# Performance work log

Hardware: AMD Instinct MI355X
Metric: run time of the kernel (lower is better)

The kernel has to match this reference:

```python
import jax, jax.numpy as jnp
import numpy as np

NUM_CLASSES = 3
STRIDES = (8, 16, 32)


def _decode(out, stride):
    # out: [B, 5+C, H, W] -> [B, H*W, 5+C] decoded to image coords; also return grid [H*W, 2]
    B, C, H, W = out.shape
    yv, xv = jnp.meshgrid(jnp.arange(H), jnp.arange(W), indexing='ij')
    grid = jnp.stack([xv, yv], -1).reshape(H * W, 2).astype(out.dtype)
    o = out.reshape(B, C, H * W).transpose(0, 2, 1)
    xy = (o[..., :2] + grid[None]) * stride
    wh = jnp.exp(o[..., 2:4]) * stride
    return jnp.concatenate([xy, wh, o[..., 4:]], -1), grid


def _pairwise_iou(gt, pr):
    # gt [G,4], pr [A,4], cxcywh -> iou [G,A]
    tl = jnp.maximum(gt[:, None, :2] - gt[:, None, 2:] / 2, pr[None, :, :2] - pr[None, :, 2:] / 2)
    br = jnp.minimum(gt[:, None, :2] + gt[:, None, 2:] / 2, pr[None, :, :2] + pr[None, :, 2:] / 2)
    en = (tl < br).all(-1).astype(gt.dtype)
    area_i = jnp.prod(br - tl, -1) * en
    area_u = jnp.prod(gt[:, None, 2:], -1) + jnp.prod(pr[None, :, 2:], -1) - area_i
    return area_i / (area_u + 1e-16)


def _iou_loss(pred, target):
    # elementwise IOUloss (loss_type='iou'): 1 - iou^2, shapes [..., 4]
    tl = jnp.maximum(pred[..., :2] - pred[..., 2:] / 2, target[..., :2] - target[..., 2:] / 2)
    br = jnp.minimum(pred[..., :2] + pred[..., 2:] / 2, target[..., :2] + target[..., 2:] / 2)
    en = (tl < br).all(-1).astype(pred.dtype)
    area_i = jnp.prod(br - tl, -1) * en
    area_u = jnp.prod(pred[..., 2:], -1) + jnp.prod(target[..., 2:], -1) - area_i
    iou = area_i / (area_u + 1e-16)
    return 1.0 - iou ** 2


def _bce_logits(x, y):
    # stable BCEWithLogits, reduction='none'
    return jnp.maximum(x, 0) - x * y + jnp.log1p(jnp.exp(-jnp.abs(x)))


def _assign(gt_boxes, gt_cls, box_p, cls_p, obj_p, xs, ys, strides):
    # SimOTA for one image. gt_boxes [G,4], gt_cls [G], box_p [A,4], cls_p [A,C], obj_p [A,1]
    G = gt_boxes.shape[0]
    C = cls_p.shape[-1]
    xc = (xs + 0.5) * strides  # [A] anchor centers in image coords
    yc = (ys + 0.5) * strides
    # anchors inside gt boxes
    gl = gt_boxes[:, 0:1] - gt_boxes[:, 2:3] / 2
    gr = gt_boxes[:, 0:1] + gt_boxes[:, 2:3] / 2
    gt_ = gt_boxes[:, 1:2] - gt_boxes[:, 3:4] / 2
    gb = gt_boxes[:, 1:2] + gt_boxes[:, 3:4] / 2
    in_box = (xc[None] > gl) & (xc[None] < gr) & (yc[None] > gt_) & (yc[None] < gb)  # [G,A]
    # anchors inside center radius 2.5 * stride
    r = 2.5
    in_ctr = ((xc[None] > gt_boxes[:, 0:1] - r * strides[None]) &
              (xc[None] < gt_boxes[:, 0:1] + r * strides[None]) &
              (yc[None] > gt_boxes[:, 1:2] - r * strides[None]) &
              (yc[None] < gt_boxes[:, 1:2] + r * strides[None]))
    cand = in_box.any(0) | in_ctr.any(0)  # [A] candidate anchors (fg_mask)
    in_both = in_box & in_ctr  # [G,A]
    ious = jnp.where(cand[None], _pairwise_iou(gt_boxes, box_p), 0.0)
    iou_cost = -jnp.log(ious + 1e-8)
    p = jnp.sqrt(jax.nn.sigmoid(cls_p) * jax.nn.sigmoid(obj_p))  # [A,C]
    y = jax.nn.one_hot(gt_cls, C, dtype=p.dtype)  # [G,C]
    cls_cost = -(jnp.einsum('gc,ac->ga', y, jnp.log(p + 1e-8)) +
                 jnp.einsum('gc,ac->ga', 1 - y, jnp.log(1 - p + 1e-8)))
    cost = cls_cost + 3.0 * iou_cost + 1e5 * (~in_both).astype(p.dtype)
    cost = jnp.where(cand[None], cost, 1e9)
    # dynamic-k: k_g = clamp(int(sum of top-10 ious), 1)
    topk_ious, _ = jax.lax.top_k(ious, 10)
    dyn_k = jnp.clip(topk_ious.sum(-1).astype(jnp.int32), 1, None)  # [G]
    ranks = jnp.argsort(jnp.argsort(cost, axis=1), axis=1)
    matching = (ranks < dyn_k[:, None]) & cand[None]  # [G,A]
    # resolve anchors matched to multiple gts by min cost
    multi = matching.sum(0) > 1  # [A]
    best = jnp.arange(G)[:, None] == jnp.argmin(cost, axis=0)[None]  # [G,A]
    matching = jnp.where(multi[None], best, matching)
    fg = matching.any(0)  # [A]
    matched_gt = jnp.argmax(matching, axis=0)  # [A]
    pred_iou = (matching.astype(p.dtype) * ious).sum(0)  # [A]
    cls_t = jax.nn.one_hot(gt_cls[matched_gt], C, dtype=p.dtype) * pred_iou[:, None]  # [A,C]
    reg_t = gt_boxes[matched_gt]  # [A,4]
    return fg, cls_t, reg_t


def _forward(p3, p4, p5, mask_inputs, labels, input_images, mask_labels, now_epoch):
    outs, grids, str_list = [], [], []
    for o, s in zip((p3, p4, p5), STRIDES):
        dec, g = _decode(o, float(s))
        outs.append(dec)
        grids.append(g)
        str_list.append(jnp.full((g.shape[0],), float(s), dtype=dec.dtype))
    outputs = jnp.concatenate(outs, 1)  # [B, A, 5+C]
    xs = jnp.concatenate([g[:, 0] for g in grids], 0)  # [A]
    ys = jnp.concatenate([g[:, 1] for g in grids], 0)
    strides = jnp.concatenate(str_list, 0)
    box_p = outputs[..., :4]
    obj_p = outputs[..., 4:5]
    cls_p = outputs[..., 5:]
    gt_boxes = labels[..., :4]
    gt_cls = labels[..., 4].astype(jnp.int32)
    fg, cls_t, reg_t = jax.vmap(_assign, in_axes=(0, 0, 0, 0, 0, None, None, None))(
        gt_boxes, gt_cls, box_p, cls_p, obj_p, xs, ys, strides)
    # assignment is @torch.no_grad() in the original
    fg, cls_t, reg_t = jax.lax.stop_gradient((fg, cls_t, reg_t))
    fgf = fg.astype(outputs.dtype)  # [B,A]
    num_fg = jnp.maximum(fgf.sum(), 1.0)
    loss_iou = (_iou_loss(box_p, reg_t) * fgf).sum()
    loss_obj = _bce_logits(obj_p[..., 0], fgf).sum()
    loss_cls = (_bce_logits(cls_p, cls_t) * fgf[..., None]).sum()
    # segmentation losses: CE (mean NLL over pixels) + Dice
    logp = jax.nn.log_softmax(mask_inputs, axis=1)  # [B,C,H,W]
    ce = -jnp.take_along_axis(logp, mask_labels[:, None].astype(jnp.int32), axis=1).mean()
    sm = jax.nn.softmax(mask_inputs, axis=1).transpose(0, 2, 3, 1)  # [B,H,W,C]
    oh = jax.nn.one_hot(mask_labels, NUM_CLASSES + 1, dtype=sm.dtype)[..., :NUM_CLASSES]
    tp = (oh * sm).sum((0, 1, 2))
    fp = sm.sum((0, 1, 2)) - tp
    fn = oh.sum((0, 1, 2)) - tp
    smooth = 1e-5
    dice = 1.0 - jnp.mean((2 * tp + smooth) / (2 * tp + fn + fp + smooth))  # beta=1
    loss_mask = ce + dice
    loss_sc = jnp.zeros((), outputs.dtype)  # is_sc=False
    reg_w = 5.0
    total = (reg_w * loss_iou + loss_obj + loss_cls + loss_sc) / num_fg + loss_mask
    return jnp.stack([total, reg_w * loss_iou / num_fg, loss_obj / num_fg,
                      loss_cls / num_fg, loss_mask, loss_sc / num_fg])


def setup_inputs() -> dict:
    key = jax.random.key(0)
    ks = jax.random.split(key, 8)
    B, IMG, G = 8, 1024, 20
    C5 = NUM_CLASSES + 5
    p3 = jax.random.normal(ks[0], (B, C5, 128, 128), jnp.float32)
    p4 = jax.random.normal(ks[1], (B, C5, 64, 64), jnp.float32)
    p5 = jax.random.normal(ks[2], (B, C5, 32, 32), jnp.float32)
    mask_inputs = jax.random.normal(ks[3], (B, NUM_CLASSES, IMG, IMG), jnp.float32)
    cxy = jax.random.uniform(ks[4], (B, G, 2), jnp.float32, 64.0, float(IMG - 64))
    wh = jax.random.uniform(ks[5], (B, G, 2), jnp.float32, 16.0, 256.0)
    cls = jax.random.randint(ks[6], (B, G, 1), 0, NUM_CLASSES).astype(jnp.float32)
    labels = jnp.concatenate([cxy, wh, cls], -1)  # [B,G,5] (cx,cy,w,h,class)
    input_images = jax.random.uniform(ks[7], (B, 1, IMG, IMG), jnp.float32)
    mask_labels = jax.random.randint(jax.random.fold_in(key, 9), (B, IMG, IMG), 0, NUM_CLASSES)
    return {"p3": p3, "p4": p4, "p5": p5, "mask_inputs": mask_inputs,
            "labels": labels, "input_images": input_images,
            "mask_labels": mask_labels, "now_epoch": 0}


def reference(p3, p4, p5, mask_inputs, labels, input_images, mask_labels, now_epoch):
    return _forward(p3, p4, p5, mask_inputs, labels, input_images, mask_labels, now_epoch)
```

## Files before the change

kernel.cpp:

```cpp
#include <hip/hip_runtime.h>
#include <cfloat>

constexpr int A_TOT = 21504;
constexpr int NB    = 8;
constexpr int NG    = 20;
constexpr int HW_M  = 1 << 20;
constexpr int SPLIT = 16;
constexpr int CHUNK = A_TOT / SPLIT;
constexpr int MBLK  = 2048;

constexpr float L2E = 1.44269504088896340736f;
constexpr float LN2 = 0.69314718055994530942f;

constexpr size_t OFF_DEC  = 0;
constexpr size_t SZ_DEC   = (size_t)NB * A_TOT * 8;
constexpr size_t OFF_IOUS = OFF_DEC + SZ_DEC;
constexpr size_t SZ_GA    = (size_t)NB * NG * A_TOT;
constexpr size_t OFF_COST = OFF_IOUS + SZ_GA;
constexpr size_t OFF_THRC = OFF_COST + SZ_GA;
constexpr size_t OFF_THRI = OFF_THRC + NB * NG;
constexpr size_t OFF_CAND = OFF_THRI + NB * NG;
constexpr size_t OFF_PM   = OFF_CAND + (NB * A_TOT) / 4;
constexpr size_t OFF_PK   = OFF_PM + 672 * 4;
constexpr size_t OFF_PV   = OFF_PK + (size_t)MBLK * 10;
constexpr size_t SZ_PART  = (size_t)NB * NG * SPLIT * 10;
constexpr size_t OFF_PC   = OFF_PV + SZ_PART;
constexpr size_t OFF_PI   = OFF_PC + SZ_PART;

__device__ __forceinline__ float hw_exp2(float x) { return __builtin_amdgcn_exp2f(x); }
__device__ __forceinline__ float hw_log2(float x) { return __builtin_amdgcn_logf(x); }
__device__ __forceinline__ float fexp(float x) { return hw_exp2(x * L2E); }
__device__ __forceinline__ float flog(float x) { return hw_log2(x) * LN2; }
__device__ __forceinline__ float frcp(float x) { return __builtin_amdgcn_rcpf(x); }
__device__ __forceinline__ float fsig(float x) { return frcp(1.f + fexp(-x)); }
__device__ __forceinline__ float fbce(float x, float y) {
  float t = hw_exp2(-fabsf(x) * L2E);
  return fmaxf(x, 0.f) - x * y + LN2 * hw_log2(1.f + t);
}
__device__ __forceinline__ void anchor_geom(int a, int& hw, int& lw, float& st) {
  if (a < 16384)      { hw = a;         lw = 7; st = 8.f;  }
  else if (a < 20480) { hw = a - 16384; lw = 6; st = 16.f; }
  else                { hw = a - 20480; lw = 5; st = 32.f; }
}

__device__ __forceinline__ void merge_desc(float* a, const float* b) {
  float m[16];
  m[0] = a[0]; m[1] = a[1]; m[2] = a[2]; m[3] = a[3]; m[4] = a[4]; m[5] = a[5];
  m[6] = fmaxf(a[6], b[9]); m[7] = fmaxf(a[7], b[8]);
  m[8] = fmaxf(a[8], b[7]); m[9] = fmaxf(a[9], b[6]);
  m[10] = b[5]; m[11] = b[4]; m[12] = b[3]; m[13] = b[2]; m[14] = b[1]; m[15] = b[0];
#pragma unroll
  for (int s = 8; s >= 1; s >>= 1) {
#pragma unroll
    for (int i = 0; i < 16; ++i) {
      if (!(i & s)) {
        float hi = fmaxf(m[i], m[i + s]);
        float lo = fminf(m[i], m[i + s]);
        m[i] = hi; m[i + s] = lo;
      }
    }
  }
#pragma unroll
  for (int j = 0; j < 10; ++j) a[j] = m[j];
}

__device__ __forceinline__ void merge_asc(float* ac, int* ai,
                                          const float* bc, const int* bi) {
  float mc[16]; int mi[16];
#pragma unroll
  for (int i = 0; i < 6; ++i) { mc[i] = ac[i]; mi[i] = ai[i]; }
#pragma unroll
  for (int i = 6; i < 10; ++i) {
    float c2 = bc[15 - i]; int i2 = bi[15 - i];
    bool ta = (ac[i] < c2) || (ac[i] == c2 && ai[i] < i2);
    mc[i] = ta ? ac[i] : c2; mi[i] = ta ? ai[i] : i2;
  }
  mc[10] = bc[5]; mi[10] = bi[5]; mc[11] = bc[4]; mi[11] = bi[4];
  mc[12] = bc[3]; mi[12] = bi[3]; mc[13] = bc[2]; mi[13] = bi[2];
  mc[14] = bc[1]; mi[14] = bi[1]; mc[15] = bc[0]; mi[15] = bi[0];
#pragma unroll
  for (int s = 8; s >= 1; s >>= 1) {
#pragma unroll
    for (int i = 0; i < 16; ++i) {
      if (!(i & s)) {
        float cA = mc[i], cB = mc[i + s];
        int   iA = mi[i], iB = mi[i + s];
        bool ta = (cB < cA) || (cB == cA && iB < iA);
        mc[i]     = ta ? cB : cA; mi[i]     = ta ? iB : iA;
        mc[i + s] = ta ? cA : cB; mi[i + s] = ta ? iA : iB;
      }
    }
  }
#pragma unroll
  for (int j = 0; j < 10; ++j) { ac[j] = mc[j]; ai[j] = mi[j]; }
}

__global__ __launch_bounds__(256) void k_cost(
    const float* __restrict__ p3, const float* __restrict__ p4,
    const float* __restrict__ p5, const float* __restrict__ labels,
    float* __restrict__ dec, float* __restrict__ ious,
    float* __restrict__ cost, unsigned char* __restrict__ cand) {
  __shared__ float gt[NG][5];
  int tid = threadIdx.x, b = blockIdx.y;
  if (tid < NG * 5) ((float*)gt)[tid] = labels[b * NG * 5 + tid];
  __syncthreads();
  int a = blockIdx.x * 256 + tid;

  int hw, lw; float st;
  anchor_geom(a, hw, lw, st);
  const float* src; int HW;
  if (a < 16384)      { src = p3; HW = 16384; }
  else if (a < 20480) { src = p4; HW = 4096;  }
  else                { src = p5; HW = 1024;  }
  int x = hw & ((1 << lw) - 1), y = hw >> lw;
  const float* c0 = src + (size_t)b * 8 * HW + hw;
  float o0 = c0[0];
  float o1 = c0[(size_t)HW];
  float o2 = c0[(size_t)2 * HW];
  float o3 = c0[(size_t)3 * HW];
  float o4 = c0[(size_t)4 * HW];
  float o5 = c0[(size_t)5 * HW];
  float o6 = c0[(size_t)6 * HW];
  float o7 = c0[(size_t)7 * HW];
  float px = (o0 + (float)x) * st, py = (o1 + (float)y) * st;
  float pw = fexp(o2) * st,        ph = fexp(o3) * st;
  {
    float4* dst = (float4*)(dec + ((size_t)b * A_TOT + a) * 8);
    dst[0] = make_float4(px, py, pw, ph);
    dst[1] = make_float4(o4, o5, o6, o7);
  }

  float xc = ((float)x + 0.5f) * st, yc = ((float)y + 0.5f) * st;

  float so = fsig(o4);
  float cc0, cc1, cc2, S;
  {
    float q0 = sqrtf(fsig(o5) * so);
    float q1 = sqrtf(fsig(o6) * so);
    float q2 = sqrtf(fsig(o7) * so);
    float lg0 = flog(q0 + 1e-8f), lg1 = flog(q1 + 1e-8f), lg2 = flog(q2 + 1e-8f);
    float m0 = flog(1.f - q0 + 1e-8f), m1 = flog(1.f - q1 + 1e-8f), m2 = flog(1.f - q2 + 1e-8f);
    S = m0 + m1 + m2;
    cc0 = lg0 - m0; cc1 = lg1 - m1; cc2 = lg2 - m2;
  }

  float iouv[NG];
  unsigned bothMask = 0;
  bool anyBox = false, anyCtr = false;
  float hpw = pw * 0.5f, hph = ph * 0.5f;
  float plx = px - hpw, prx = px + hpw, pty = py - hph, pby = py + hph;
  float parea = pw * ph;
  float r = 2.5f * st;

#pragma unroll
  for (int g = 0; g < NG; ++g) {
    float gx = gt[g][0], gy = gt[g][1], gw = gt[g][2], gh = gt[g][3];
    float hgw = gw * 0.5f, hgh = gh * 0.5f;
    float glx = gx - hgw, grx = gx + hgw, gty = gy - hgh, gby = gy + hgh;
    bool ib = (xc > glx) && (xc < grx) && (yc > gty) && (yc < gby);
    bool ic = (xc > gx - r) && (xc < gx + r) && (yc > gy - r) && (yc < gy + r);
    anyBox |= ib; anyCtr |= ic;
    if (ib && ic) bothMask |= (1u << g);
    float tlx = fmaxf(glx, plx), brx = fminf(grx, prx);
    float tly = fmaxf(gty, pty), bry = fminf(gby, pby);
    float en = ((tlx < brx) && (tly < bry)) ? 1.f : 0.f;
    float ai = (brx - tlx) * (bry - tly) * en;
    float au = gw * gh + parea - ai;
    iouv[g] = ai / (au + 1e-16f);
  }
  bool cd = anyBox || anyCtr;
  cand[(size_t)b * A_TOT + a] = cd ? 1 : 0;

#pragma unroll
  for (int g = 0; g < NG; ++g) {
    float iv = cd ? iouv[g] : 0.f;
    int cg = (int)gt[g][4];
    float ccg = (cg == 0) ? cc0 : ((cg == 1) ? cc1 : cc2);
    float c = -(ccg + S) - 3.f * flog(iv + 1e-8f) +
              (((bothMask >> g) & 1u) ? 0.f : 100000.f);
    size_t idx = ((size_t)(b * NG + g)) * A_TOT + a;
    ious[idx] = iv;
    cost[idx] = cd ? c : 1e9f;
  }
}

__global__ __launch_bounds__(64) void k_topk_part(
    const float* __restrict__ ious, const float* __restrict__ cost,
    float* __restrict__ pV, float* __restrict__ pC, int* __restrict__ pI) {
  int s = blockIdx.x, g = blockIdx.y, b = blockIdx.z;
  int lane = threadIdx.x;
  int row = b * NG + g;
  int lo = s * CHUNK;
  const float4* iou4 = (const float4*)(ious + (size_t)row * A_TOT + lo);
  const float4* cst4 = (const float4*)(cost + (size_t)row * A_TOT + lo);
  constexpr int NG4 = CHUNK / 4;

  float tv[10];
  float tc[10]; int ti[10];
#pragma unroll
  for (int j = 0; j < 10; ++j) { tv[j] = -1e30f; tc[j] = FLT_MAX; ti[j] = 0x7fffffff; }

  auto insV = [&](float v) {
    if (v > tv[9]) {
#pragma unroll
      for (int j = 0; j < 10; ++j)
        if (v > tv[j]) { float t = tv[j]; tv[j] = v; v = t; }
    }
  };
  auto insC = [&](float c, int ii) {
    if ((c < tc[9]) || (c == tc[9] && ii < ti[9])) {
#pragma unroll
      for (int j = 0; j < 10; ++j) {
        bool lt = (c < tc[j]) || (c == tc[j] && ii < ti[j]);
        if (lt) {
          float t = tc[j]; tc[j] = c; c = t;
          int t2 = ti[j]; ti[j] = ii; ii = t2;
        }
      }
    }
  };

#pragma unroll 1
  for (int grp = lane; grp < NG4; grp += 64) {
    float4 v4 = iou4[grp];
    float4 c4 = cst4[grp];
    int base = lo + grp * 4;
    insV(v4.x); insV(v4.y); insV(v4.z); insV(v4.w);
    insC(c4.x, base); insC(c4.y, base + 1); insC(c4.z, base + 2); insC(c4.w, base + 3);
  }

#pragma unroll 1
  for (int d = 1; d < 64; d <<= 1) {
    float bv[10];
#pragma unroll
    for (int j = 0; j < 10; ++j) bv[j] = __shfl_xor(tv[j], d, 64);
    merge_desc(tv, bv);
  }
#pragma unroll 1
  for (int d = 1; d < 64; d <<= 1) {
    float bc[10]; int bi[10];
#pragma unroll
    for (int j = 0; j < 10; ++j) {
      bc[j] = __shfl_xor(tc[j], d, 64);
      bi[j] = __shfl_xor(ti[j], d, 64);
    }
    merge_asc(tc, ti, bc, bi);
  }

  if (lane == 0) {
    size_t base = ((size_t)row * SPLIT + s) * 10;
#pragma unroll
    for (int j = 0; j < 10; ++j) {
      pV[base + j] = tv[j];
      pC[base + j] = tc[j];
      pI[base + j] = ti[j];
    }
  }
}

__global__ __launch_bounds__(192) void k_topk_merge(
    const float* __restrict__ pV, const float* __restrict__ pC,
    const int* __restrict__ pI, float* __restrict__ thrC, int* __restrict__ thrI) {
  int g = blockIdx.x, b = blockIdx.y, tid = threadIdx.x;
  int row = b * NG + g;
  constexpr int NC = SPLIT * 10;
  __shared__ float sV[NC], sC[NC];
  __shared__ int   sI[NC];
  __shared__ float slot[10];
  __shared__ int kS;

  if (tid < NC) {
    size_t base = (size_t)row * NC + tid;
    sV[tid] = pV[base];
    sC[tid] = pC[base];
    sI[tid] = pI[base];
  }
  __syncthreads();

  float myV = 0.f, myC = 0.f; int myI = 0, rankV = 0;
  if (tid < NC) {
    myV = sV[tid]; myC = sC[tid]; myI = sI[tid];
    for (int j = 0; j < NC; ++j) {
      float v = sV[j];
      rankV += ((v > myV) || (v == myV && j < tid)) ? 1 : 0;
    }
  }
  if (tid < NC && rankV < 10) slot[rankV] = myV;
  __syncthreads();
  if (tid == 0) {
    float sum = 0.f;
#pragma unroll
    for (int j = 0; j < 10; ++j) sum += slot[j];
    int k = (int)sum; if (k < 1) k = 1;
    kS = k;
  }
  __syncthreads();
  if (tid < NC) {
    int rankC = 0;
    for (int j = 0; j < NC; ++j) {
      float c = sC[j];
      rankC += ((c < myC) || (c == myC && sI[j] < myI)) ? 1 : 0;
    }
    if (rankC == kS - 1) { thrC[row] = myC; thrI[row] = myI; }
  }
}

__global__ __launch_bounds__(256) void k_match(
    const float* __restrict__ dec, const float* __restrict__ labels,
    const float* __restrict__ ious, const float* __restrict__ cost,
    const unsigned char* __restrict__ cand,
    const float* __restrict__ thrC, const int* __restrict__ thrI,
    float* __restrict__ pm) {
  __shared__ float gt[NG][5];
  __shared__ float tC[NG];
  __shared__ int   tI[NG];
  int tid = threadIdx.x, b = blockIdx.y;
  if (tid < NG * 5) ((float*)gt)[tid] = labels[b * NG * 5 + tid];
  if (tid >= 128 && tid < 128 + NG) tC[tid - 128] = thrC[b * NG + tid - 128];
  if (tid >= 160 && tid < 160 + NG) tI[tid - 160] = thrI[b * NG + tid - 160];
  __syncthreads();
  int a = blockIdx.x * 256 + tid;

  bool cd = cand[(size_t)b * A_TOT + a] != 0;
  int cnt = 0, firstg = -1, gmin = 0;
  float minc = FLT_MAX, pisum = 0.f, iou_gmin = 0.f;
#pragma unroll
  for (int g = 0; g < NG; ++g) {
    size_t idx = ((size_t)(b * NG + g)) * A_TOT + a;
    float c = cost[idx];
    float iv = ious[idx];
    if (c < minc) { minc = c; gmin = g; iou_gmin = iv; }
    bool m = cd && ((c < tC[g]) || (c == tC[g] && a <= tI[g]));
    if (m) { cnt++; if (firstg < 0) firstg = g; pisum += iv; }
  }
  if (cnt > 1) { firstg = gmin; pisum = iou_gmin; }
  bool fg = cnt > 0;

  const float4* dp = (const float4*)(dec + ((size_t)b * A_TOT + a) * 8);
  float4 d0 = dp[0], d1 = dp[1];
  float l_obj = fbce(d1.x, fg ? 1.f : 0.f);
  float l_iou = 0.f, l_cls = 0.f, nfg = fg ? 1.f : 0.f;
  if (fg) {
    float gx = gt[firstg][0], gy = gt[firstg][1];
    float gw = gt[firstg][2], gh = gt[firstg][3];
    int cg = (int)gt[firstg][4];
    float px = d0.x, py = d0.y, pw = d0.z, ph = d0.w;
    float tlx = fmaxf(px - pw * 0.5f, gx - gw * 0.5f);
    float brx = fminf(px + pw * 0.5f, gx + gw * 0.5f);
    float tly = fmaxf(py - ph * 0.5f, gy - gh * 0.5f);
    float bry = fminf(py + ph * 0.5f, gy + gh * 0.5f);
    float en = ((tlx < brx) && (tly < bry)) ? 1.f : 0.f;
    float ai = (brx - tlx) * (bry - tly) * en;
    float au = pw * ph + gw * gh - ai;
    float iou = ai / (au + 1e-16f);
    l_iou = 1.f - iou * iou;
    l_cls  = fbce(d1.y, (cg == 0) ? pisum : 0.f);
    l_cls += fbce(d1.z, (cg == 1) ? pisum : 0.f);
    l_cls += fbce(d1.w, (cg == 2) ? pisum : 0.f);
  }

  __shared__ float scr[4][4];
  float vals[4] = { nfg, l_iou, l_obj, l_cls };
#pragma unroll
  for (int k = 0; k < 4; ++k) {
    float v = vals[k];
#pragma unroll
    for (int off = 32; off > 0; off >>= 1) v += __shfl_down(v, off, 64);
    if ((tid & 63) == 0) scr[tid >> 6][k] = v;
  }
  __syncthreads();
  if (tid == 0) {
    int bf = blockIdx.y * gridDim.x + blockIdx.x;
#pragma unroll
    for (int k = 0; k < 4; ++k)
      pm[(size_t)bf * 4 + k] = scr[0][k] + scr[1][k] + scr[2][k] + scr[3][k];
  }
}

__global__ __launch_bounds__(256) void k_mask(
    const float* __restrict__ mi, const int* __restrict__ ml,
    float* __restrict__ pk) {
  int tid = threadIdx.x;
  int blk = blockIdx.x;
  int b  = blk >> 8;
  int g0 = (blk & 255) << 10;
  const float* base0 = mi + (size_t)b * 3 * HW_M + (size_t)g0 * 4;
  const int*   lbase = ml + ((size_t)b << 20) + (size_t)g0 * 4;

  float4 x0[4], x1[4], x2[4]; int4 lb[4];
#pragma unroll
  for (int u = 0; u < 4; ++u) {
    size_t off = (size_t)(tid + u * 256) * 4;
    x0[u] = *(const float4*)(base0 + off);
    x1[u] = *(const float4*)(base0 + HW_M + off);
    x2[u] = *(const float4*)(base0 + 2 * HW_M + off);
    lb[u] = *(const int4*)(lbase + off);
  }

  float ce = 0.f, tp0 = 0, tp1 = 0, tp2 = 0;
  float ss0 = 0, ss1 = 0;
  float c0 = 0, c1 = 0;

  auto proc = [&](float v0, float v1, float v2, int l) {
    float e0 = hw_exp2(v0 * L2E);
    float e1 = hw_exp2(v1 * L2E);
    float e2 = hw_exp2(v2 * L2E);
    float sum = e0 + e1 + e2;
    float inv = __builtin_amdgcn_rcpf(sum);
    float lse = hw_log2(sum) * LN2;
    float s0 = e0 * inv, s1 = e1 * inv;
    ss0 += s0; ss1 += s1;
    bool l0 = (l == 0), l1 = (l == 1);
    float vl = l0 ? v0 : (l1 ? v1 : v2);
    float el = l0 ? e0 : (l1 ? e1 : e2);
    float sl = el * inv;
    ce += vl - lse;
    tp0 += l0 ? sl : 0.f;
    tp1 += l1 ? sl : 0.f;
    tp2 += (!l0 && !l1) ? sl : 0.f;
    c0 += l0 ? 1.f : 0.f;
    c1 += l1 ? 1.f : 0.f;
  };

#pragma unroll
  for (int u = 0; u < 4; ++u) {
    proc(x0[u].x, x1[u].x, x2[u].x, lb[u].x);
    proc(x0[u].y, x1[u].y, x2[u].y, lb[u].y);
    proc(x0[u].z, x1[u].z, x2[u].z, lb[u].z);
    proc(x0[u].w, x1[u].w, x2[u].w, lb[u].w);
  }
  float ss2 = 16.f - ss0 - ss1;
  float c2 = 16.f - c0 - c1;

  __shared__ float scr[4][10];
  float vals[10] = { ce, tp0, tp1, tp2, ss0, ss1, ss2, c0, c1, c2 };
#pragma unroll
  for (int k = 0; k < 10; ++k) {
    float v = vals[k];
#pragma unroll
    for (int off = 32; off > 0; off >>= 1) v += __shfl_down(v, off, 64);
    if ((tid & 63) == 0) scr[tid >> 6][k] = v;
  }
  __syncthreads();
  if (tid == 0) {
#pragma unroll
    for (int k = 0; k < 10; ++k)
      pk[(size_t)blk * 10 + k] = scr[0][k] + scr[1][k] + scr[2][k] + scr[3][k];
  }
}

__device__ __forceinline__ float bsum256(float v, float* scr) {
#pragma unroll
  for (int off = 32; off > 0; off >>= 1) v += __shfl_down(v, off, 64);
  __syncthreads();
  if ((threadIdx.x & 63) == 0) scr[threadIdx.x >> 6] = v;
  __syncthreads();
  return scr[0] + scr[1] + scr[2] + scr[3];
}

__global__ __launch_bounds__(256) void k_final(
    const float* __restrict__ pm, const float* __restrict__ pk,
    float* __restrict__ out) {
  __shared__ float scr[4];
  int tid = threadIdx.x;
  float t0 = 0, t1 = 0, t2 = 0, t3 = 0;
  for (int r = tid; r < 672; r += 256) {
    t0 += pm[(size_t)r * 4 + 0];
    t1 += pm[(size_t)r * 4 + 1];
    t2 += pm[(size_t)r * 4 + 2];
    t3 += pm[(size_t)r * 4 + 3];
  }
  float u[10] = {0,0,0,0,0,0,0,0,0,0};
  for (int r = tid; r < MBLK; r += 256) {
#pragma unroll
    for (int k = 0; k < 10; ++k) u[k] += pk[(size_t)r * 10 + k];
  }
  float S_nfg = bsum256(t0, scr);
  float S_iou = bsum256(t1, scr);
  float S_obj = bsum256(t2, scr);
  float S_cls = bsum256(t3, scr);
  float S_ce  = bsum256(u[0], scr);
  float S_tp0 = bsum256(u[1], scr);
  float S_tp1 = bsum256(u[2], scr);
  float S_tp2 = bsum256(u[3], scr);
  float S_ss0 = bsum256(u[4], scr);
  float S_ss1 = bsum256(u[5], scr);
  float S_ss2 = bsum256(u[6], scr);
  float S_c0  = bsum256(u[7], scr);
  float S_c1  = bsum256(u[8], scr);
  float S_c2  = bsum256(u[9], scr);

  if (tid == 0) {
    float nfg = fmaxf(S_nfg, 1.f);
    float o1 = 5.f * S_iou / nfg;
    float o2 = S_obj / nfg;
    float o3 = S_cls / nfg;
    float ce = -S_ce / (float)((long long)NB << 20);
    float tps[3] = { S_tp0, S_tp1, S_tp2 };
    float sss[3] = { S_ss0, S_ss1, S_ss2 };
    float cns[3] = { S_c0, S_c1, S_c2 };
    float ds = 0.f;
#pragma unroll
    for (int c = 0; c < 3; ++c) {
      float tp = tps[c];
      float fp = sss[c] - tp;
      float fn = cns[c] - tp;
      ds += (2.f * tp + 1e-5f) / (2.f * tp + fn + fp + 1e-5f);
    }
    float dice = 1.f - ds / 3.f;
    float o4 = ce + dice;
    out[0] = o1 + o2 + o3 + o4;
    out[1] = o1;
    out[2] = o2;
    out[3] = o3;
    out[4] = o4;
    out[5] = 0.f;
  }
}

extern "C" void kernel_launch(void* const* d_in, const int* in_sizes, int n_in,
                              void* d_out, int out_size, void* d_ws, size_t ws_size,
                              hipStream_t stream) {
  const float* p3     = (const float*)d_in[0];
  const float* p4     = (const float*)d_in[1];
  const float* p5     = (const float*)d_in[2];
  const float* mi     = (const float*)d_in[3];
  const float* labels = (const float*)d_in[4];
  const int*   ml     = (const int*)d_in[6];

  float* ws   = (float*)d_ws;
  float* dec  = ws + OFF_DEC;
  float* ious = ws + OFF_IOUS;
  float* cost = ws + OFF_COST;
  float* thrC = ws + OFF_THRC;
  int*   thrI = (int*)(ws + OFF_THRI);
  unsigned char* cand = (unsigned char*)(ws + OFF_CAND);
  float* pm   = ws + OFF_PM;
  float* pk   = ws + OFF_PK;
  float* pV   = ws + OFF_PV;
  float* pC   = ws + OFF_PC;
  int*   pI   = (int*)(ws + OFF_PI);
  float* out  = (float*)d_out;

  dim3 gA(A_TOT / 256, NB);
  k_cost<<<gA, 256, 0, stream>>>(p3, p4, p5, labels, dec, ious, cost, cand);
  k_topk_part<<<dim3(SPLIT, NG, NB), 64, 0, stream>>>(ious, cost, pV, pC, pI);
  k_topk_merge<<<dim3(NG, NB), 192, 0, stream>>>(pV, pC, pI, thrC, thrI);
  k_match<<<gA, 256, 0, stream>>>(dec, labels, ious, cost, cand, thrC, thrI, pm);
  k_mask<<<MBLK, 256, 0, stream>>>(mi, ml, pk);
  k_final<<<1, 256, 0, stream>>>(pm, pk, out);
}
```

Before: 104.5 us.

## Split independent mask-loss work across the four detection kernels to fill idle CUs

Removes the standalone mask kernel and splits its 2048 blocks into four slices. Each slice rides as extra blocks on one of the detection-loss kernels (cost, top-k partial, top-k merge, match), so the small, latency-bound detection stages share the GPU with bandwidth-heavy mask work instead of leaving CUs idle. The top-k partial kernel also packs four 64-thread wavefronts per 256-thread block. This removes one launch but adds branch divergence between block roles and may raise register or LDS pressure for the fused kernels.

```diff
diff --git a/kernel.cpp b/kernel.cpp
--- a/kernel.cpp
+++ b/kernel.cpp
@@ -8,6 +8,7 @@
 constexpr int SPLIT = 16;
 constexpr int CHUNK = A_TOT / SPLIT;
 constexpr int MBLK  = 2048;
+constexpr int MSLC  = MBLK / 4;
 
 constexpr float L2E = 1.44269504088896340736f;
 constexpr float LN2 = 0.69314718055994530942f;
@@ -95,16 +96,90 @@
   for (int j = 0; j < 10; ++j) { ac[j] = mc[j]; ai[j] = mi[j]; }
 }
 
-__global__ __launch_bounds__(256) void k_cost(
+__device__ __forceinline__ void mask_block(int vblk,
+    const float* __restrict__ mi, const int* __restrict__ ml,
+    float* __restrict__ pk, int tid) {
+  int b  = vblk >> 8;
+  int g0 = (vblk & 255) << 10;
+  const float* base0 = mi + (size_t)b * 3 * HW_M + (size_t)g0 * 4;
+  const int*   lbase = ml + ((size_t)b << 20) + (size_t)g0 * 4;
+
+  float4 x0[4], x1[4], x2[4]; int4 lb[4];
+#pragma unroll
+  for (int u = 0; u < 4; ++u) {
+    size_t off = (size_t)(tid + u * 256) * 4;
+    x0[u] = *(const float4*)(base0 + off);
+    x1[u] = *(const float4*)(base0 + HW_M + off);
+    x2[u] = *(const float4*)(base0 + 2 * HW_M + off);
+    lb[u] = *(const int4*)(lbase + off);
+  }
+
+  float ce = 0.f, tp0 = 0, tp1 = 0, tp2 = 0;
+  float ss0 = 0, ss1 = 0, c0 = 0, c1 = 0;
+
+  auto proc = [&](float v0, float v1, float v2, int l) {
+    float e0 = hw_exp2(v0 * L2E);
+    float e1 = hw_exp2(v1 * L2E);
+    float e2 = hw_exp2(v2 * L2E);
+    float sum = e0 + e1 + e2;
+    float inv = __builtin_amdgcn_rcpf(sum);
+    float lse = hw_log2(sum) * LN2;
+    float s0 = e0 * inv, s1 = e1 * inv;
+    ss0 += s0; ss1 += s1;
+    bool l0 = (l == 0), l1 = (l == 1);
+    float vl = l0 ? v0 : (l1 ? v1 : v2);
+    float el = l0 ? e0 : (l1 ? e1 : e2);
+    float sl = el * inv;
+    ce += vl - lse;
+    tp0 += l0 ? sl : 0.f;
+    tp1 += l1 ? sl : 0.f;
+    tp2 += (!l0 && !l1) ? sl : 0.f;
+    c0 += l0 ? 1.f : 0.f;
+    c1 += l1 ? 1.f : 0.f;
+  };
+
+#pragma unroll
+  for (int u = 0; u < 4; ++u) {
+    proc(x0[u].x, x1[u].x, x2[u].x, lb[u].x);
+    proc(x0[u].y, x1[u].y, x2[u].y, lb[u].y);
+    proc(x0[u].z, x1[u].z, x2[u].z, lb[u].z);
+    proc(x0[u].w, x1[u].w, x2[u].w, lb[u].w);
+  }
+  float ss2 = 16.f - ss0 - ss1;
+  float c2 = 16.f - c0 - c1;
+
+  __shared__ float scr[4][10];
+  float vals[10] = { ce, tp0, tp1, tp2, ss0, ss1, ss2, c0, c1, c2 };
+#pragma unroll
+  for (int k = 0; k < 10; ++k) {
+    float v = vals[k];
+#pragma unroll
+    for (int off = 32; off > 0; off >>= 1) v += __shfl_down(v, off, 64);
+    if ((tid & 63) == 0) scr[tid >> 6][k] = v;
+  }
+  __syncthreads();
+  if (tid == 0) {
+#pragma unroll
+    for (int k = 0; k < 10; ++k)
+      pk[(size_t)vblk * 10 + k] = scr[0][k] + scr[1][k] + scr[2][k] + scr[3][k];
+  }
+}
+
+__global__ __launch_bounds__(256) void k_cost_mask(
     const float* __restrict__ p3, const float* __restrict__ p4,
     const float* __restrict__ p5, const float* __restrict__ labels,
     float* __restrict__ dec, float* __restrict__ ious,
-    float* __restrict__ cost, unsigned char* __restrict__ cand) {
+    float* __restrict__ cost, unsigned char* __restrict__ cand,
+    const float* __restrict__ mi, const int* __restrict__ ml,
+    float* __restrict__ pk) {
+  int bi = blockIdx.x, tid = threadIdx.x;
+  if (bi >= 672) { mask_block(bi - 672, mi, ml, pk, tid); return; }
+  int b = bi / 84, cx = bi - b * 84;
+
   __shared__ float gt[NG][5];
-  int tid = threadIdx.x, b = blockIdx.y;
   if (tid < NG * 5) ((float*)gt)[tid] = labels[b * NG * 5 + tid];
   __syncthreads();
-  int a = blockIdx.x * 256 + tid;
+  int a = cx * 256 + tid;
 
   int hw, lw; float st;
   anchor_geom(a, hw, lw, st);
@@ -184,11 +259,20 @@
   }
 }
 
-__global__ __launch_bounds__(64) void k_topk_part(
+__global__ __launch_bounds__(256) void k_topk_mask(
     const float* __restrict__ ious, const float* __restrict__ cost,
-    float* __restrict__ pV, float* __restrict__ pC, int* __restrict__ pI) {
-  int s = blockIdx.x, g = blockIdx.y, b = blockIdx.z;
-  int lane = threadIdx.x;
+    float* __restrict__ pV, float* __restrict__ pC, int* __restrict__ pI,
+    const float* __restrict__ mi, const int* __restrict__ ml,
+    float* __restrict__ pk) {
+  int bi = blockIdx.x, tid = threadIdx.x;
+  if (bi >= 640) { mask_block(MSLC + (bi - 640), mi, ml, pk, tid); return; }
+
+  int w = tid >> 6, lane = tid & 63;
+  int t = bi * 4 + w;
+  int b = t / (NG * SPLIT);
+  int rem = t - b * (NG * SPLIT);
+  int g = rem / SPLIT;
+  int s = rem - g * SPLIT;
   int row = b * NG + g;
   int lo = s * CHUNK;
   const float4* iou4 = (const float4*)(ious + (size_t)row * A_TOT + lo);
@@ -204,7 +288,7 @@
     if (v > tv[9]) {
 #pragma unroll
       for (int j = 0; j < 10; ++j)
-        if (v > tv[j]) { float t = tv[j]; tv[j] = v; v = t; }
+        if (v > tv[j]) { float t2 = tv[j]; tv[j] = v; v = t2; }
     }
   };
   auto insC = [&](float c, int ii) {
@@ -213,8 +297,8 @@
       for (int j = 0; j < 10; ++j) {
         bool lt = (c < tc[j]) || (c == tc[j] && ii < ti[j]);
         if (lt) {
-          float t = tc[j]; tc[j] = c; c = t;
-          int t2 = ti[j]; ti[j] = ii; ii = t2;
+          float t2 = tc[j]; tc[j] = c; c = t2;
+          int t3 = ti[j]; ti[j] = ii; ii = t3;
         }
       }
     }
@@ -238,13 +322,13 @@
   }
 #pragma unroll 1
   for (int d = 1; d < 64; d <<= 1) {
-    float bc[10]; int bi[10];
+    float bc[10]; int bi2[10];
 #pragma unroll
     for (int j = 0; j < 10; ++j) {
       bc[j] = __shfl_xor(tc[j], d, 64);
-      bi[j] = __shfl_xor(ti[j], d, 64);
-    }
-    merge_asc(tc, ti, bc, bi);
+      bi2[j] = __shfl_xor(ti[j], d, 64);
+    }
+    merge_asc(tc, ti, bc, bi2);
   }
 
   if (lane == 0) {
@@ -258,11 +342,14 @@
   }
 }
 
-__global__ __launch_bounds__(192) void k_topk_merge(
+__global__ __launch_bounds__(256) void k_merge_mask(
     const float* __restrict__ pV, const float* __restrict__ pC,
-    const int* __restrict__ pI, float* __restrict__ thrC, int* __restrict__ thrI) {
-  int g = blockIdx.x, b = blockIdx.y, tid = threadIdx.x;
-  int row = b * NG + g;
+    const int* __restrict__ pI, float* __restrict__ thrC, int* __restrict__ thrI,
+    const float* __restrict__ mi, const int* __restrict__ ml,
+    float* __restrict__ pk) {
+  int bi = blockIdx.x, tid = threadIdx.x;
+  if (bi >= 160) { mask_block(2 * MSLC + (bi - 160), mi, ml, pk, tid); return; }
+  int row = bi;
   constexpr int NC = SPLIT * 10;
   __shared__ float sV[NC], sC[NC];
   __shared__ int   sI[NC];
@@ -305,21 +392,26 @@
   }
 }
 
-__global__ __launch_bounds__(256) void k_match(
+__global__ __launch_bounds__(256) void k_match_mask(
     const float* __restrict__ dec, const float* __restrict__ labels,
     const float* __restrict__ ious, const float* __restrict__ cost,
     const unsigned char* __restrict__ cand,
     const float* __restrict__ thrC, const int* __restrict__ thrI,
-    float* __restrict__ pm) {
+    float* __restrict__ pm,
+    const float* __restrict__ mi, const int* __restrict__ ml,
+    float* __restrict__ pk) {
+  int bi = blockIdx.x, tid = threadIdx.x;
+  if (bi >= 672) { mask_block(3 * MSLC + (bi - 672), mi, ml, pk, tid); return; }
+  int b = bi / 84, cx = bi - b * 84;
+
   __shared__ float gt[NG][5];
   __shared__ float tC[NG];
   __shared__ int   tI[NG];
-  int tid = threadIdx.x, b = blockIdx.y;
   if (tid < NG * 5) ((float*)gt)[tid] = labels[b * NG * 5 + tid];
   if (tid >= 128 && tid < 128 + NG) tC[tid - 128] = thrC[b * NG + tid - 128];
   if (tid >= 160 && tid < 160 + NG) tI[tid - 160] = thrI[b * NG + tid - 160];
   __syncthreads();
-  int a = blockIdx.x * 256 + tid;
+  int a = cx * 256 + tid;
 
   bool cd = cand[(size_t)b * A_TOT + a] != 0;
   int cnt = 0, firstg = -1, gmin = 0;
@@ -359,93 +451,20 @@
     l_cls += fbce(d1.w, (cg == 2) ? pisum : 0.f);
   }
 
-  __shared__ float scr[4][4];
+  __shared__ float scr2[4][4];
   float vals[4] = { nfg, l_iou, l_obj, l_cls };
 #pragma unroll
   for (int k = 0; k < 4; ++k) {
     float v = vals[k];
 #pragma unroll
     for (int off = 32; off > 0; off >>= 1) v += __shfl_down(v, off, 64);
-    if ((tid & 63) == 0) scr[tid >> 6][k] = v;
+    if ((tid & 63) == 0) scr2[tid >> 6][k] = v;
   }
   __syncthreads();
   if (tid == 0) {
-    int bf = blockIdx.y * gridDim.x + blockIdx.x;
 #pragma unroll
     for (int k = 0; k < 4; ++k)
-      pm[(size_t)bf * 4 + k] = scr[0][k] + scr[1][k] + scr[2][k] + scr[3][k];
-  }
-}
-
-__global__ __launch_bounds__(256) void k_mask(
-    const float* __restrict__ mi, const int* __restrict__ ml,
-    float* __restrict__ pk) {
-  int tid = threadIdx.x;
-  int blk = blockIdx.x;
-  int b  = blk >> 8;
-  int g0 = (blk & 255) << 10;
-  const float* base0 = mi + (size_t)b * 3 * HW_M + (size_t)g0 * 4;
-  const int*   lbase = ml + ((size_t)b << 20) + (size_t)g0 * 4;
-
-  float4 x0[4], x1[4], x2[4]; int4 lb[4];
-#pragma unroll
-  for (int u = 0; u < 4; ++u) {
-    size_t off = (size_t)(tid + u * 256) * 4;
-    x0[u] = *(const float4*)(base0 + off);
-    x1[u] = *(const float4*)(base0 + HW_M + off);
-    x2[u] = *(const float4*)(base0 + 2 * HW_M + off);
-    lb[u] = *(const int4*)(lbase + off);
-  }
-
-  float ce = 0.f, tp0 = 0, tp1 = 0, tp2 = 0;
-  float ss0 = 0, ss1 = 0;
-  float c0 = 0, c1 = 0;
-
-  auto proc = [&](float v0, float v1, float v2, int l) {
-    float e0 = hw_exp2(v0 * L2E);
-    float e1 = hw_exp2(v1 * L2E);
-    float e2 = hw_exp2(v2 * L2E);
-    float sum = e0 + e1 + e2;
-    float inv = __builtin_amdgcn_rcpf(sum);
-    float lse = hw_log2(sum) * LN2;
-    float s0 = e0 * inv, s1 = e1 * inv;
-    ss0 += s0; ss1 += s1;
-    bool l0 = (l == 0), l1 = (l == 1);
-    float vl = l0 ? v0 : (l1 ? v1 : v2);
-    float el = l0 ? e0 : (l1 ? e1 : e2);
-    float sl = el * inv;
-    ce += vl - lse;
-    tp0 += l0 ? sl : 0.f;
-    tp1 += l1 ? sl : 0.f;
-    tp2 += (!l0 && !l1) ? sl : 0.f;
-    c0 += l0 ? 1.f : 0.f;
-    c1 += l1 ? 1.f : 0.f;
-  };
-
-#pragma unroll
-  for (int u = 0; u < 4; ++u) {
-    proc(x0[u].x, x1[u].x, x2[u].x, lb[u].x);
-    proc(x0[u].y, x1[u].y, x2[u].y, lb[u].y);
-    proc(x0[u].z, x1[u].z, x2[u].z, lb[u].z);
-    proc(x0[u].w, x1[u].w, x2[u].w, lb[u].w);
-  }
-  float ss2 = 16.f - ss0 - ss1;
-  float c2 = 16.f - c0 - c1;
-
-  __shared__ float scr[4][10];
-  float vals[10] = { ce, tp0, tp1, tp2, ss0, ss1, ss2, c0, c1, c2 };
-#pragma unroll
-  for (int k = 0; k < 10; ++k) {
-    float v = vals[k];
-#pragma unroll
-    for (int off = 32; off > 0; off >>= 1) v += __shfl_down(v, off, 64);
-    if ((tid & 63) == 0) scr[tid >> 6][k] = v;
-  }
-  __syncthreads();
-  if (tid == 0) {
-#pragma unroll
-    for (int k = 0; k < 10; ++k)
-      pk[(size_t)blk * 10 + k] = scr[0][k] + scr[1][k] + scr[2][k] + scr[3][k];
+      pm[(size_t)bi * 4 + k] = scr2[0][k] + scr2[1][k] + scr2[2][k] + scr2[3][k];
   }
 }
 
@@ -542,11 +561,13 @@
   int*   pI   = (int*)(ws + OFF_PI);
   float* out  = (float*)d_out;
 
-  dim3 gA(A_TOT / 256, NB);
-  k_cost<<<gA, 256, 0, stream>>>(p3, p4, p5, labels, dec, ious, cost, cand);
-  k_topk_part<<<dim3(SPLIT, NG, NB), 64, 0, stream>>>(ious, cost, pV, pC, pI);
-  k_topk_merge<<<dim3(NG, NB), 192, 0, stream>>>(pV, pC, pI, thrC, thrI);
-  k_match<<<gA, 256, 0, stream>>>(dec, labels, ious, cost, cand, thrC, thrI, pm);
-  k_mask<<<MBLK, 256, 0, stream>>>(mi, ml, pk);
+  k_cost_mask <<<672 + MSLC, 256, 0, stream>>>(p3, p4, p5, labels, dec, ious,
+                                               cost, cand, mi, ml, pk);
+  k_topk_mask <<<640 + MSLC, 256, 0, stream>>>(ious, cost, pV, pC, pI,
+                                               mi, ml, pk);
+  k_merge_mask<<<160 + MSLC, 256, 0, stream>>>(pV, pC, pI, thrC, thrI,
+                                               mi, ml, pk);
+  k_match_mask<<<672 + MSLC, 256, 0, stream>>>(dec, labels, ious, cost, cand,
+                                               thrC, thrI, pm, mi, ml, pk);
   k_final<<<1, 256, 0, stream>>>(pm, pk, out);
 }
```

After: 91.40 us (median of 4 runs). -12.5%, faster.
